# Performance work log

Measured on AMD Instinct MI355X. Metric: run time of the kernel, lower is better.

Reference implementation:

```python
import jax, jax.numpy as jnp
import numpy as np

N_HEADS = 8
CLIP = 10.0  # tanh clipping constant of the pointer logits
NEG = -1e9


def setup_inputs() -> dict:
    key = jax.random.key(0)
    ks = jax.random.split(key, 10)
    B, N, H = 1024, 100, 128
    s = 1.0 / np.sqrt(H).astype(np.float32)
    return {
        "encoder_inputs": jax.random.normal(ks[0], (B, N, H), jnp.float32),
        "pool": jax.random.normal(ks[1], (B, H), jnp.float32),
        "capacity": jnp.full((B, 1), 50.0, jnp.float32),  # vehicle capacity
        "demand": (1.0 + 9.0 * jax.random.uniform(ks[2], (B, N), jnp.float32)).at[:, 0].set(0.0),  # depot demand = 0
        "fc_w": jax.random.normal(ks[3], (H, H + 1), jnp.float32) * s,
        "fc1_w": jax.random.normal(ks[4], (H, H), jnp.float32) * s,
        "Wq": jax.random.normal(ks[5], (H, H), jnp.float32) * s,
        "Wk": jax.random.normal(ks[6], (H, H), jnp.float32) * s,
        "Wv": jax.random.normal(ks[7], (H, H), jnp.float32) * s,
        "Wo": jax.random.normal(ks[8], (H, H), jnp.float32) * s,
        "Wk2": jax.random.normal(ks[9], (H, H), jnp.float32) * s,
        "n_steps": 128,
        "T": 1,
        "greedy": 1,
    }


def _decode(encoder_inputs, pool, capacity, demand, fc_w, fc1_w, Wq, Wk, Wv, Wo, Wk2, n_steps, T):
    B, N, H = encoder_inputs.shape
    hd = H // N_HEADS
    # encoder projections are step-invariant -> hoist out of the loop
    K = (encoder_inputs @ Wk.T).reshape(B, N, N_HEADS, hd)
    V = (encoder_inputs @ Wv.T).reshape(B, N, N_HEADS, hd)
    K2 = encoder_inputs @ Wk2.T  # [B, N, H] pointer keys
    pool_proj = pool @ fc1_w.T   # [B, H]
    base_cap = capacity[0, 0]
    rows = jnp.arange(B)

    def update_mask(cap, index, mask1):
        # mask1: permanently visited customers (depot never permanently masked)
        go_depot = (index == 0)
        mask1 = mask1.at[rows, index].set(1.0)
        mask1 = mask1.at[:, 0].set(0.0)
        mask = jnp.maximum(mask1, (demand > cap).astype(jnp.float32))
        # cannot stay at depot; but depot must stay open once all customers are masked
        all_cust = jnp.all(mask[:, 1:] > 0.0, axis=1)
        depot = jnp.where(all_cust, 0.0, go_depot.astype(jnp.float32))
        mask = mask.at[:, 0].set(depot)
        return mask, mask1

    mask0, mask1_0 = update_mask(capacity, jnp.zeros((B,), jnp.int32), jnp.zeros((B, N), jnp.float32))
    inp0 = encoder_inputs[:, 0, :]
    inv_sqrt_hd = 1.0 / jnp.sqrt(jnp.float32(hd))
    inv_sqrt_h = 1.0 / jnp.sqrt(jnp.float32(H))

    def step(carry, _):
        _inp, cap, mask, mask1 = carry
        dec = jnp.concatenate([_inp, cap], axis=-1) @ fc_w.T + pool_proj  # [B, H]
        # multi-head glimpse over encoder nodes
        q = (dec @ Wq.T).reshape(B, N_HEADS, hd)
        scores = jnp.einsum('bhd,bnhd->bhn', q, K) * inv_sqrt_hd
        scores = jnp.where(mask[:, None, :] > 0.0, NEG, scores)
        attn = jax.nn.softmax(scores, axis=-1)
        glimpse = jnp.einsum('bhn,bnhd->bhd', attn, V).reshape(B, H) @ Wo.T
        # single-head clipped pointer logits
        u = CLIP * jnp.tanh(jnp.einsum('bh,bnh->bn', glimpse, K2) * inv_sqrt_h)
        u = jnp.where(mask > 0.0, NEG, u)
        logp_all = jax.nn.log_softmax(u / T, axis=-1)
        index = jnp.argmax(logp_all, axis=-1)  # greedy decoding
        log_p = jnp.take_along_axis(logp_all, index[:, None], axis=1)[:, 0]
        is_done = (jnp.sum(mask1[:, 1:], axis=1) >= N - 1).astype(jnp.float32)
        log_p = log_p * (1.0 - is_done)
        # state update: subtract served demand; reset to base capacity at depot
        sel_d = jnp.take_along_axis(demand, index[:, None], axis=1)
        cap = jnp.where(index[:, None] == 0, base_cap, cap - sel_d)
        mask, mask1 = update_mask(cap, index, mask1)
        _inp = jnp.take_along_axis(encoder_inputs, index[:, None, None], axis=1)[:, 0]
        return (_inp, cap, mask, mask1), (index, log_p)

    _, (actions, log_ps) = jax.lax.scan(step, (inp0, capacity, mask0, mask1_0), None, length=n_steps)
    return actions.T, jnp.sum(log_ps, axis=0)  # ([B, n_steps], [B])


def reference(encoder_inputs, pool, capacity, demand, fc_w, fc1_w, Wq, Wk, Wv, Wo, Wk2, n_steps, T, greedy):
    actions, log_p = _decode(encoder_inputs, pool, capacity, demand, fc_w, fc1_w, Wq, Wk, Wv, Wo, Wk2, n_steps, T)
    return actions, log_p
```

## Files before the change

### kernel.cpp

```cpp
#include <hip/hip_runtime.h>
#include <math.h>

#define NNODE 100
#define NEGV  -1000000000.0f

__device__ float g_Wall [128 * 512];
__device__ float g_Wall2[128 * 128];
__device__ float g_qcap [128];
__device__ float g_C    [(size_t)102400 * 512];
__device__ float g_qpool[(size_t)1024 * 128];
__device__ float g_S1   [(size_t)1024 * 100 * 800];
__device__ float g_Scap [(size_t)1024 * 800];

__device__ __forceinline__ float fast_rcp(float x) { return __builtin_amdgcn_rcpf(x); }
__device__ __forceinline__ float tanh10(float z) {
    const float e2 = __expf(2.0f * z);
    return fmaf(-20.0f, __builtin_amdgcn_rcpf(e2 + 1.0f), 10.0f);
}
__device__ __forceinline__ unsigned fkey(float v) {
    const unsigned u = __float_as_uint(v);
    return (u & 0x80000000u) ? ~u : (u | 0x80000000u);
}
__device__ __forceinline__ float funkey(unsigned k) {
    return __uint_as_float((k & 0x80000000u) ? (k ^ 0x80000000u) : ~k);
}

template<int CTRL>
__device__ __forceinline__ int dpp_i(int v) {
    return __builtin_amdgcn_update_dpp(0, v, CTRL, 0xF, 0xF, true);
}
template<int CTRL>
__device__ __forceinline__ float dpp_f(float v) {
    return __uint_as_float((unsigned)dpp_i<CTRL>(__float_as_int(v)));
}
__device__ __forceinline__ float swz16_f(float v) {
    return __uint_as_float(
        (unsigned)__builtin_amdgcn_ds_swizzle(__float_as_int(v), 0x401F));
}

__global__ __launch_bounds__(128) void prep_kernel(
    const float* __restrict__ Wk,  const float* __restrict__ Wv,
    const float* __restrict__ Wk2, const float* __restrict__ Wo,
    const float* __restrict__ Wq,  const float* __restrict__ fc_w,
    const float* __restrict__ fc1_w)
{
    const int c = blockIdx.x;
    const int k = threadIdx.x;
    if (c < 128) {
        g_Wall[k * 512 + c] = Wk[c * 128 + k];
    } else if (c < 256) {
        g_Wall[k * 512 + c] = Wv[(c - 128) * 128 + k];
    } else if (c < 384) {
        const int cc = c - 256;
        float acc = 0.f;
        for (int h = 0; h < 128; h++)
            acc = fmaf(Wk2[h * 128 + k], Wo[h * 128 + cc], acc);
        g_Wall[k * 512 + c] = acc;
    } else if (c < 512) {
        const int cc = c - 384;
        float acc = 0.f;
        for (int j = 0; j < 128; j++)
            acc = fmaf(Wq[cc * 128 + j], fc_w[j * 129 + k], acc);
        g_Wall[k * 512 + c] = acc;
    } else if (c == 512) {
        float acc = 0.f;
        for (int j = 0; j < 128; j++)
            acc = fmaf(Wq[k * 128 + j], fc_w[j * 129 + 128], acc);
        g_qcap[k] = acc;
    } else {
        const int cc = c - 513;
        float acc = 0.f;
        for (int j = 0; j < 128; j++)
            acc = fmaf(Wq[cc * 128 + j], fc1_w[j * 128 + k], acc);
        g_Wall2[k * 128 + cc] = acc;
    }
}

__global__ __launch_bounds__(256) void gemm_kernel(const float* __restrict__ A,
                                                   int mode)
{
    const float* __restrict__ W = mode ? g_Wall2 : g_Wall;
    float* __restrict__ C       = mode ? g_qpool : g_C;
    const int ncols             = mode ? 128 : 512;
    const int m0 = blockIdx.x * 128, n0 = blockIdx.y * 128;

    __shared__ __align__(16) float At[32 * 132];
    __shared__ __align__(16) float Ws[32 * 128];
    const int tid = threadIdx.x;
    const int tm = tid >> 5, tn = tid & 31;
    const int mb = tm * 16, nb = tn * 4;
    float4 acc[16];
#pragma unroll
    for (int i = 0; i < 16; i++) acc[i] = make_float4(0.f, 0.f, 0.f, 0.f);

    for (int kc = 0; kc < 4; kc++) {
        for (int f = tid; f < 1024; f += 256) {
            const int r = f >> 3, q8 = f & 7;
            float4 a = *(const float4*)&A[(size_t)(m0 + r) * 128 + kc * 32 + q8 * 4];
            At[(q8 * 4 + 0) * 132 + r] = a.x;
            At[(q8 * 4 + 1) * 132 + r] = a.y;
            At[(q8 * 4 + 2) * 132 + r] = a.z;
            At[(q8 * 4 + 3) * 132 + r] = a.w;
            const int kl = f >> 5, q = f & 31;
            *(float4*)&Ws[kl * 128 + q * 4] =
                *(const float4*)&W[(size_t)(kc * 32 + kl) * ncols + n0 + q * 4];
        }
        __syncthreads();
        for (int k = 0; k < 32; k++) {
            const float4 w = *(float4*)&Ws[k * 128 + nb];
#pragma unroll
            for (int i = 0; i < 16; i += 4) {
                const float4 a = *(float4*)&At[k * 132 + mb + i];
                acc[i + 0].x = fmaf(a.x, w.x, acc[i + 0].x);
                acc[i + 0].y = fmaf(a.x, w.y, acc[i + 0].y);
                acc[i + 0].z = fmaf(a.x, w.z, acc[i + 0].z);
                acc[i + 0].w = fmaf(a.x, w.w, acc[i + 0].w);
                acc[i + 1].x = fmaf(a.y, w.x, acc[i + 1].x);
                acc[i + 1].y = fmaf(a.y, w.y, acc[i + 1].y);
                acc[i + 1].z = fmaf(a.y, w.z, acc[i + 1].z);
                acc[i + 1].w = fmaf(a.y, w.w, acc[i + 1].w);
                acc[i + 2].x = fmaf(a.z, w.x, acc[i + 2].x);
                acc[i + 2].y = fmaf(a.z, w.y, acc[i + 2].y);
                acc[i + 2].z = fmaf(a.z, w.z, acc[i + 2].z);
                acc[i + 2].w = fmaf(a.z, w.w, acc[i + 2].w);
                acc[i + 3].x = fmaf(a.w, w.x, acc[i + 3].x);
                acc[i + 3].y = fmaf(a.w, w.y, acc[i + 3].y);
                acc[i + 3].z = fmaf(a.w, w.z, acc[i + 3].z);
                acc[i + 3].w = fmaf(a.w, w.w, acc[i + 3].w);
            }
        }
        __syncthreads();
    }
#pragma unroll
    for (int i = 0; i < 16; i++)
        *(float4*)&C[(size_t)(m0 + mb + i) * ncols + n0 + nb] = acc[i];
}

__global__ __launch_bounds__(256) void s1_kernel()
{
    const int b = blockIdx.x;
    const int tid = threadIdx.x;
    const int h = tid >> 5, l32 = tid & 31;
    const float* __restrict__ Crow = &g_C[(size_t)b * 100 * 512];

    __shared__ __align__(16) float Q1sh[NNODE * 128];
    for (int f = tid; f < 3200; f += 256) {
        const int n = f >> 5, c4 = f & 31;
        *(float4*)&Q1sh[n * 128 + c4 * 4] =
            *(const float4*)&Crow[(size_t)n * 512 + 384 + c4 * 4];
    }
    __syncthreads();

    float4 kr[4][4];
    int nn[4];
#pragma unroll
    for (int j = 0; j < 4; j++) {
        nn[j] = l32 + 32 * j;
#pragma unroll
        for (int i = 0; i < 4; i++) {
            kr[j][i] = (nn[j] < 100)
                ? *(const float4*)&Crow[(size_t)nn[j] * 512 + h * 16 + i * 4]
                : make_float4(0.f, 0.f, 0.f, 0.f);
        }
    }
    float4 qc[4], qp[4];
#pragma unroll
    for (int i = 0; i < 4; i++) {
        qc[i] = *(const float4*)&g_qcap[h * 16 + i * 4];
        qp[i] = *(const float4*)&g_qpool[(size_t)b * 128 + h * 16 + i * 4];
    }
    float sp[4];
#pragma unroll
    for (int j = 0; j < 4; j++) {
        float dc = 0.f, dp = 0.f;
#pragma unroll
        for (int i = 0; i < 4; i++) {
            dc = fmaf(kr[j][i].x, qc[i].x, dc); dc = fmaf(kr[j][i].y, qc[i].y, dc);
            dc = fmaf(kr[j][i].z, qc[i].z, dc); dc = fmaf(kr[j][i].w, qc[i].w, dc);
            dp = fmaf(kr[j][i].x, qp[i].x, dp); dp = fmaf(kr[j][i].y, qp[i].y, dp);
            dp = fmaf(kr[j][i].z, qp[i].z, dp); dp = fmaf(kr[j][i].w, qp[i].w, dp);
        }
        sp[j] = dp;
        if (nn[j] < 100)
            g_Scap[(size_t)b * 800 + h * 100 + nn[j]] = dc * 0.25f;
    }

    float* __restrict__ S1b = &g_S1[(size_t)b * 80000];
    for (int m = 0; m < 100; m++) {
        float4 q[4];
#pragma unroll
        for (int i = 0; i < 4; i++)
            q[i] = *(float4*)&Q1sh[m * 128 + h * 16 + i * 4];
#pragma unroll
        for (int j = 0; j < 4; j++) {
            if (nn[j] < 100) {
                float d = 0.f;
#pragma unroll
                for (int i = 0; i < 4; i++) {
                    d = fmaf(kr[j][i].x, q[i].x, d); d = fmaf(kr[j][i].y, q[i].y, d);
                    d = fmaf(kr[j][i].z, q[i].z, d); d = fmaf(kr[j][i].w, q[i].w, d);
                }
                S1b[(size_t)m * 800 + h * 100 + nn[j]] = (d + sp[j]) * 0.25f;
            }
        }
    }
}

__global__ __launch_bounds__(256) void decode_kernel(
    const float* __restrict__ capacity, const float* __restrict__ demand,
    const int* __restrict__ nsteps_p, const int* __restrict__ T_p,
    float* __restrict__ out)
{
    __shared__ float u_buf[2 * 800];
    __shared__ float demand_sh[NNODE];
    __shared__ int   act_sh[512];

    const int tid = threadIdx.x;
    const int b   = blockIdx.x;
    const int nsteps = nsteps_p[0];
    const float invT = 1.0f / (float)T_p[0];
    const float base_cap = capacity[0];
    const float inv_sqrt_h = 0.08838834764831845f;

    const float4* __restrict__ C4  = (const float4*)&g_C[(size_t)b * 100 * 512];
    const float*  __restrict__ S1b = &g_S1[(size_t)b * 80000];

    const int w = tid >> 6, l = tid & 63;
    const int g = l >> 3, f = l & 7;
    const int F = 8 * w + f;
    const int h8 = tid >> 5, l32 = tid & 31;

    float4 Vreg[13], K2r[13];
#pragma unroll
    for (int m = 0; m < 13; m++) {
        const int n = g + 8 * m;
        const bool v = n < 100;
        Vreg[m] = v ? C4[(size_t)n * 128 + 32 + F] : make_float4(0.f, 0.f, 0.f, 0.f);
        K2r[m]  = v ? C4[(size_t)n * 128 + 64 + F] : make_float4(0.f, 0.f, 0.f, 0.f);
    }
    float s1r[4], scapr[4], d4[4];
#pragma unroll
    for (int j = 0; j < 4; j++) {
        const int nj = l32 + 32 * j;
        const bool v = nj < 100;
        scapr[j] = v ? g_Scap[(size_t)b * 800 + h8 * 100 + nj] : 0.f;
        s1r[j]   = v ? S1b[h8 * 100 + nj] : 0.f;
        d4[j]    = v ? demand[b * 100 + nj] : 1.0e30f;
    }
    const float de0 = demand[b * 100 + l];
    const float de1 = (l + 64 < 100) ? demand[b * 100 + l + 64] : 1.0e30f;
    for (int n = tid; n < 100; n += 256) demand_sh[n] = demand[b * 100 + n];
    bool me0 = false, me1 = false;
    unsigned mb4 = 0;
    float cap_r = capacity[b];
    float depot_r;
    {
        const bool am0 = (l == 0) ? true : (de0 > cap_r);
        const bool am1 = (l + 64 >= 100) ? true : (de1 > cap_r);
        depot_r = __all(am0 && am1) ? 0.f : 1.f;
    }
    float logp_r = 0.f;
    int visited_r = 0;
    int ub = 0;
    __syncthreads();

    for (int s = 0; s < nsteps; s++) {
        const float cap = cap_r;

        float a[4];
        float tot;
        {
            float sc[4];
#pragma unroll
            for (int j = 0; j < 4; j++) {
                const int nj = l32 + 32 * j;
                const bool m = (nj == 0) ? (depot_r != 0.f)
                    : (((mb4 >> j) & 1u) || (d4[j] > cap));
                const float raw = fmaf(cap, scapr[j], s1r[j]);
                sc[j] = (nj < 100 && !m) ? raw : NEGV;
            }
#pragma unroll
            for (int j = 0; j < 4; j++) a[j] = __expf(sc[j]);
            tot = (a[0] + a[1]) + (a[2] + a[3]);
        }

        float4 gp4 = make_float4(0.f, 0.f, 0.f, 0.f);
#pragma unroll
        for (int m = 0; m < 13; m++) {
            const int src = ((f >> 2) << 5) | (8 * (m & 3) + g);
            const float av = __shfl(a[m >> 2], src, 64);
            gp4.x = fmaf(av, Vreg[m].x, gp4.x);
            gp4.y = fmaf(av, Vreg[m].y, gp4.y);
            gp4.z = fmaf(av, Vreg[m].z, gp4.z);
            gp4.w = fmaf(av, Vreg[m].w, gp4.w);
        }
        tot += dpp_f<0xB1>(tot);
        tot += dpp_f<0x4E>(tot);
        tot += dpp_f<0x124>(tot);
        tot += dpp_f<0x128>(tot);
        tot += swz16_f(tot);
        gp4.x += dpp_f<0x128>(gp4.x);
        gp4.y += dpp_f<0x128>(gp4.y);
        gp4.z += dpp_f<0x128>(gp4.z);
        gp4.w += dpp_f<0x128>(gp4.w);
        gp4.x += swz16_f(gp4.x);
        gp4.y += swz16_f(gp4.y);
        gp4.z += swz16_f(gp4.z);
        gp4.w += swz16_f(gp4.w);
        gp4.x += __shfl_xor(gp4.x, 32, 64);
        gp4.y += __shfl_xor(gp4.y, 32, 64);
        gp4.z += __shfl_xor(gp4.z, 32, 64);
        gp4.w += __shfl_xor(gp4.w, 32, 64);
        {
            const float th = __shfl(tot, ((f >> 2) << 5) | l32, 64);
            const float rt = fast_rcp(th);
            gp4.x *= rt; gp4.y *= rt; gp4.z *= rt; gp4.w *= rt;
        }

        {
            float pm[13];
#pragma unroll
            for (int m = 0; m < 13; m++) {
                float p = gp4.x * K2r[m].x;
                p = fmaf(gp4.y, K2r[m].y, p);
                p = fmaf(gp4.z, K2r[m].z, p);
                p = fmaf(gp4.w, K2r[m].w, p);
                pm[m] = p;
            }
#pragma unroll
            for (int m = 0; m < 13; m++) pm[m] += dpp_f<0xB1>(pm[m]);
#pragma unroll
            for (int m = 0; m < 13; m++) pm[m] += dpp_f<0x4E>(pm[m]);
            if ((f & 3) == 0) {
                const int r = w * 2 + (f >> 2);
#pragma unroll
                for (int m = 0; m < 13; m++) {
                    const int n = g + 8 * m;
                    if (n < 100) u_buf[ub + r * 100 + n] = pm[m];
                }
            }
        }
        __syncthreads();

        float v0, v1 = -3.0e38f;
        {
            float s8 = 0.f;
#pragma unroll
            for (int r = 0; r < 8; r++) s8 += u_buf[ub + r * 100 + l];
            const float u0 = tanh10(s8 * inv_sqrt_h);
            const bool m0 = (l == 0) ? (depot_r != 0.f) : (me0 || de0 > cap);
            v0 = (m0 ? NEGV : u0) * invT;
            if (l + 64 < 100) {
                float t8 = 0.f;
#pragma unroll
                for (int r = 0; r < 8; r++) t8 += u_buf[ub + r * 100 + l + 64];
                const float u1 = tanh10(t8 * inv_sqrt_h);
                const bool m1 = (me1 || de1 > cap);
                v1 = (m1 ? NEGV : u1) * invT;
            }
        }
        unsigned long long p;
        float tt;
        {
            const unsigned long long p0 =
                ((unsigned long long)fkey(v0) << 32) | (unsigned)(127 - l);
            const unsigned long long p1 =
                ((unsigned long long)fkey(v1) << 32) | (unsigned)(127 - (l + 64));
            p = (p1 > p0) ? p1 : p0;
            tt = __expf(v0) + ((l + 64 < 100) ? __expf(v1) : 0.f);
        }
#define E_DPP_STAGE(CTRL)                                                     \
        {                                                                     \
            const int lo = dpp_i<CTRL>((int)(unsigned)p);                     \
            const int hi = dpp_i<CTRL>((int)(unsigned)(p >> 32));             \
            const float tn = dpp_f<CTRL>(tt);                                 \
            const unsigned long long po =                                     \
                ((unsigned long long)(unsigned)hi << 32) | (unsigned)lo;      \
            tt += tn;                                                         \
            if (po > p) p = po;                                               \
        }
        E_DPP_STAGE(0xB1)
        E_DPP_STAGE(0x4E)
        E_DPP_STAGE(0x124)
        E_DPP_STAGE(0x128)
#undef E_DPP_STAGE
        {
            const int lo = __builtin_amdgcn_ds_swizzle((int)(unsigned)p, 0x401F);
            const int hi = __builtin_amdgcn_ds_swizzle((int)(unsigned)(p >> 32), 0x401F);
            const float tn = swz16_f(tt);
            const unsigned long long po =
                ((unsigned long long)(unsigned)hi << 32) | (unsigned)lo;
            tt += tn;
            if (po > p) p = po;
        }
        {
            const unsigned lo = __shfl_xor((unsigned)p, 32, 64);
            const unsigned hi = __shfl_xor((unsigned)(p >> 32), 32, 64);
            const float tn = __shfl_xor(tt, 32, 64);
            const unsigned long long po = ((unsigned long long)hi << 32) | lo;
            tt += tn;
            if (po > p) p = po;
        }
        const int idx = 127 - (int)(unsigned)(p & 0xffffffffULL);
        const float bv = funkey((unsigned)(p >> 32));

#pragma unroll
        for (int j = 0; j < 4; j++) {
            const int nj = l32 + 32 * j;
            if (nj < 100)
                s1r[j] = S1b[(size_t)idx * 800 + h8 * 100 + nj];
        }

        const float dmd_idx = demand_sh[idx];
        const float capn = (idx == 0) ? base_cap : (cap - dmd_idx);

        if (visited_r < 99) logp_r += bv - __logf(tt);
        visited_r += (idx > 0) ? 1 : 0;
        me0 = me0 || (l == idx && idx > 0);
        me1 = me1 || (l + 64 == idx);
#pragma unroll
        for (int j = 0; j < 4; j++)
            if ((l32 + 32 * j) == idx && idx > 0) mb4 |= (1u << j);

        const bool am0 = (l == 0) ? true : (me0 || de0 > capn);
        const bool am1 = (l + 64 >= 100) ? true : (me1 || de1 > capn);
        const bool allc = __all(am0 && am1);
        depot_r = allc ? 0.f : ((idx == 0) ? 1.f : 0.f);
        cap_r = capn;
        if (tid == 0) act_sh[s] = idx;
        ub ^= 800;
    }

    __syncthreads();
    for (int t = tid; t < nsteps; t += 256)
        out[(size_t)b * nsteps + t] = (float)act_sh[t];
    if (tid == 0)
        out[(size_t)gridDim.x * nsteps + b] = logp_r;
}

extern "C" void kernel_launch(void* const* d_in, const int* in_sizes, int n_in,
                              void* d_out, int out_size, void* d_ws, size_t ws_size,
                              hipStream_t stream) {
    const float* enc    = (const float*)d_in[0];
    const float* pool   = (const float*)d_in[1];
    const float* cap    = (const float*)d_in[2];
    const float* demand = (const float*)d_in[3];
    const float* fc_w   = (const float*)d_in[4];
    const float* fc1_w  = (const float*)d_in[5];
    const float* Wq     = (const float*)d_in[6];
    const float* Wk     = (const float*)d_in[7];
    const float* Wv     = (const float*)d_in[8];
    const float* Wo     = (const float*)d_in[9];
    const float* Wk2    = (const float*)d_in[10];
    const int*   nst    = (const int*)d_in[11];
    const int*   Tp     = (const int*)d_in[12];
    float* out = (float*)d_out;

    prep_kernel<<<641, 128, 0, stream>>>(Wk, Wv, Wk2, Wo, Wq, fc_w, fc1_w);
    gemm_kernel<<<dim3(800, 4), 256, 0, stream>>>(enc, 0);
    gemm_kernel<<<dim3(8, 1),   256, 0, stream>>>(pool, 1);
    s1_kernel<<<1024, 256, 0, stream>>>();
    decode_kernel<<<1024, 256, 0, stream>>>(cap, demand, nst, Tp, out);
}
```

Measured before the change: 853.6 us.

## Exit decode early once all customers are served; remap lanes and transpose u_buf

The decode loop now breaks once every customer has been visited and the chosen node is the depot, and zero-fills the remaining actions. After that point the reference would only keep choosing the depot with zero log-prob, so the tail steps are skipped work. Lanes are also remapped so each 32-lane half owns its own feature slice. This replaces the cross-half shuffle_xor and the broadcast of the softmax total with an extra DPP stage. The partial-logit buffer is transposed to node-major, so each node's 8 partials are read with two float4 LDS loads instead of 8 strided scalar loads.

Result: slower. 990.3 us (+16.0%).

```diff
diff --git a/kernel.cpp b/kernel.cpp
--- a/kernel.cpp
+++ b/kernel.cpp
@@ -211,7 +211,7 @@
     const int* __restrict__ nsteps_p, const int* __restrict__ T_p,
     float* __restrict__ out)
 {
-    __shared__ float u_buf[2 * 800];
+    __shared__ __align__(16) float u_buf[2 * 800];
     __shared__ float demand_sh[NNODE];
     __shared__ int   act_sh[512];
 
@@ -226,8 +226,8 @@
     const float*  __restrict__ S1b = &g_S1[(size_t)b * 80000];
 
     const int w = tid >> 6, l = tid & 63;
-    const int g = l >> 3, f = l & 7;
-    const int F = 8 * w + f;
+    const int half = l >> 5, j2 = l & 3, g = (l >> 2) & 7;
+    const int F = 8 * w + half * 4 + j2;
     const int h8 = tid >> 5, l32 = tid & 31;
 
     float4 Vreg[13], K2r[13];
@@ -262,6 +262,7 @@
     float logp_r = 0.f;
     int visited_r = 0;
     int ub = 0;
+    int sdone = nsteps;
     __syncthreads();
 
     for (int s = 0; s < nsteps; s++) {
@@ -287,7 +288,7 @@
         float4 gp4 = make_float4(0.f, 0.f, 0.f, 0.f);
 #pragma unroll
         for (int m = 0; m < 13; m++) {
-            const int src = ((f >> 2) << 5) | (8 * (m & 3) + g);
+            const int src = (half << 5) | (8 * (m & 3) + g);
             const float av = __shfl(a[m >> 2], src, 64);
             gp4.x = fmaf(av, Vreg[m].x, gp4.x);
             gp4.y = fmaf(av, Vreg[m].y, gp4.y);
@@ -299,6 +300,10 @@
         tot += dpp_f<0x124>(tot);
         tot += dpp_f<0x128>(tot);
         tot += swz16_f(tot);
+        gp4.x += dpp_f<0x124>(gp4.x);
+        gp4.y += dpp_f<0x124>(gp4.y);
+        gp4.z += dpp_f<0x124>(gp4.z);
+        gp4.w += dpp_f<0x124>(gp4.w);
         gp4.x += dpp_f<0x128>(gp4.x);
         gp4.y += dpp_f<0x128>(gp4.y);
         gp4.z += dpp_f<0x128>(gp4.z);
@@ -307,13 +312,8 @@
         gp4.y += swz16_f(gp4.y);
         gp4.z += swz16_f(gp4.z);
         gp4.w += swz16_f(gp4.w);
-        gp4.x += __shfl_xor(gp4.x, 32, 64);
-        gp4.y += __shfl_xor(gp4.y, 32, 64);
-        gp4.z += __shfl_xor(gp4.z, 32, 64);
-        gp4.w += __shfl_xor(gp4.w, 32, 64);
-        {
-            const float th = __shfl(tot, ((f >> 2) << 5) | l32, 64);
-            const float rt = fast_rcp(th);
+        {
+            const float rt = fast_rcp(tot);
             gp4.x *= rt; gp4.y *= rt; gp4.z *= rt; gp4.w *= rt;
         }
 
@@ -331,12 +331,12 @@
             for (int m = 0; m < 13; m++) pm[m] += dpp_f<0xB1>(pm[m]);
 #pragma unroll
             for (int m = 0; m < 13; m++) pm[m] += dpp_f<0x4E>(pm[m]);
-            if ((f & 3) == 0) {
-                const int r = w * 2 + (f >> 2);
+            if (j2 == 0) {
+                const int r = w * 2 + half;
 #pragma unroll
                 for (int m = 0; m < 13; m++) {
                     const int n = g + 8 * m;
-                    if (n < 100) u_buf[ub + r * 100 + n] = pm[m];
+                    if (n < 100) u_buf[ub + n * 8 + r] = pm[m];
                 }
             }
         }
@@ -344,16 +344,18 @@
 
         float v0, v1 = -3.0e38f;
         {
-            float s8 = 0.f;
-#pragma unroll
-            for (int r = 0; r < 8; r++) s8 += u_buf[ub + r * 100 + l];
+            const float4 q0 = *(float4*)&u_buf[ub + l * 8];
+            const float4 q1 = *(float4*)&u_buf[ub + l * 8 + 4];
+            const float s8 = ((q0.x + q0.y) + (q0.z + q0.w))
+                           + ((q1.x + q1.y) + (q1.z + q1.w));
             const float u0 = tanh10(s8 * inv_sqrt_h);
             const bool m0 = (l == 0) ? (depot_r != 0.f) : (me0 || de0 > cap);
             v0 = (m0 ? NEGV : u0) * invT;
             if (l + 64 < 100) {
-                float t8 = 0.f;
-#pragma unroll
-                for (int r = 0; r < 8; r++) t8 += u_buf[ub + r * 100 + l + 64];
+                const float4 t0 = *(float4*)&u_buf[ub + (l + 64) * 8];
+                const float4 t1 = *(float4*)&u_buf[ub + (l + 64) * 8 + 4];
+                const float t8 = ((t0.x + t0.y) + (t0.z + t0.w))
+                               + ((t1.x + t1.y) + (t1.z + t1.w));
                 const float u1 = tanh10(t8 * inv_sqrt_h);
                 const bool m1 = (me1 || de1 > cap);
                 v1 = (m1 ? NEGV : u1) * invT;
@@ -429,11 +431,13 @@
         cap_r = capn;
         if (tid == 0) act_sh[s] = idx;
         ub ^= 800;
+
+        if (visited_r >= 99 && idx == 0) { sdone = s; break; }
     }
 
     __syncthreads();
     for (int t = tid; t < nsteps; t += 256)
-        out[(size_t)b * nsteps + t] = (float)act_sh[t];
+        out[(size_t)b * nsteps + t] = (t <= sdone) ? (float)act_sh[t] : 0.f;
     if (tid == 0)
         out[(size_t)gridDim.x * nsteps + b] = logp_r;
 }
```
